# Kernel tuning notes

Measured on AMD Instinct MI355X. Metric: run time of the kernel, lower is better.

The kernel has to match this reference:

```python
import jax, jax.numpy as jnp
import numpy as np

N_NODES = 50000
N_EDGES = 500000
NEG_SLOPE = 0.2


def gat_conv(h, src, dst, W, attn_l, attn_r, bias, activation):
    """DGL-style GATConv (feat_drop=attn_drop=0, no residual).
    h: [N, F_in]; W: [F_in, H*D]; attn_l/attn_r: [H, D]; bias: [H*D].
    Returns [N, H, D]."""
    H, D = attn_l.shape
    feat = (h @ W).reshape(-1, H, D)                      # [N, H, D]
    el = (feat * attn_l).sum(-1)                          # [N, H]
    er = (feat * attn_r).sum(-1)                          # [N, H]
    e = jax.nn.leaky_relu(el[src] + er[dst], NEG_SLOPE)   # [E, H] edge logits
    # edge softmax over incoming edges of each dst node
    emax = jax.ops.segment_max(e, dst, num_segments=N_NODES)
    emax = jnp.where(jnp.isfinite(emax), emax, 0.0)       # guard zero in-degree
    ee = jnp.exp(e - emax[dst])                           # [E, H]
    denom = jax.ops.segment_sum(ee, dst, num_segments=N_NODES)
    alpha = ee / jnp.maximum(denom[dst], 1e-9)            # [E, H]
    # weighted scatter-aggregate of source features
    out = jax.ops.segment_sum(feat[src] * alpha[..., None], dst,
                              num_segments=N_NODES)       # [N, H, D]
    out = out + bias.reshape(1, H, D)
    return activation(out) if activation is not None else out


def setup_inputs() -> dict:
    key = jax.random.key(0)
    ks = jax.random.split(key, 20)
    in0, in1, hid, heads, ncls = 256, 128, 64, 8, 10

    def xn(k, shape):
        fan = shape[0] + (shape[1] if len(shape) > 1 else shape[0])
        return jax.random.normal(k, shape, jnp.float32) * np.float32(np.sqrt(2.0 / fan)) * 1.414

    inp = {
        "feat0": jax.random.normal(ks[0], (30000, in0), jnp.float32),
        "feat1": jax.random.normal(ks[1], (20000, in1), jnp.float32),
        "fc0_w": xn(ks[2], (in0, hid)), "fc0_b": jnp.zeros((hid,), jnp.float32),
        "fc1_w": xn(ks[3], (in1, hid)), "fc1_b": jnp.zeros((hid,), jnp.float32),
        "W0": xn(ks[4], (hid, heads * hid)),
        "al0": xn(ks[5], (heads, hid)), "ar0": xn(ks[6], (heads, hid)),
        "b0": jnp.zeros((heads * hid,), jnp.float32),
        "W1": xn(ks[7], (heads * hid, heads * hid)),
        "al1": xn(ks[8], (heads, hid)), "ar1": xn(ks[9], (heads, hid)),
        "b1": jnp.zeros((heads * hid,), jnp.float32),
        "W2": xn(ks[10], (heads * hid, 1 * ncls)),
        "al2": xn(ks[11], (1, ncls)), "ar2": xn(ks[12], (1, ncls)),
        "b2": jnp.zeros((ncls,), jnp.float32),
        "edge_index": jax.random.randint(ks[13], (2, N_EDGES), 0, N_NODES, jnp.int64
                                         if jax.config.jax_enable_x64 else jnp.int32),
    }
    return inp


def reference(feat0, feat1, fc0_w, fc0_b, fc1_w, fc1_b,
              W0, al0, ar0, b0, W1, al1, ar1, b1, W2, al2, ar2, b2,
              edge_index):
    src, dst = edge_index[0], edge_index[1]
    # per-type linear projection then concat along node axis
    h = jnp.concatenate([feat0 @ fc0_w + fc0_b, feat1 @ fc1_w + fc1_b], axis=0)
    h = gat_conv(h, src, dst, W0, al0, ar0, b0, jax.nn.elu).reshape(N_NODES, -1)
    h = gat_conv(h, src, dst, W1, al1, ar1, b1, jax.nn.elu).reshape(N_NODES, -1)
    logits = gat_conv(h, src, dst, W2, al2, ar2, b2, None).mean(axis=1)  # [N, ncls]
    return logits
```

## Files before the change

### kernel.cpp

```cpp
#include <hip/hip_runtime.h>
#include <hip/hip_bf16.h>

#define N_NODES 50000
#define N_EDGES 500000
#define HEADS 8
#define HID 64
#define HD 512
#define NCLS 10
#define M_PAD 50048

typedef __bf16 bf16x8 __attribute__((ext_vector_type(8)));
typedef float  f32x4  __attribute__((ext_vector_type(4)));
typedef unsigned short us8v __attribute__((ext_vector_type(8)));

__device__ __forceinline__ float bf2f(unsigned short u) {
    union { unsigned int i; float f; } v; v.i = ((unsigned int)u) << 16; return v.f;
}
__device__ __forceinline__ unsigned short f2bf(float x) {
    __hip_bfloat16 b = __float2bfloat16(x);
    return *reinterpret_cast<unsigned short*>(&b);
}

#define GLD_LDS16(g, l) __builtin_amdgcn_global_load_lds( \
    (__attribute__((address_space(1))) void*)(g),         \
    (__attribute__((address_space(3))) void*)(l), 16, 0, 0)

#define T0_TILES 469
#define T1_TILES 313
__global__ __launch_bounds__(256) void fc_gemm(const float* __restrict__ A0,
                                               const float* __restrict__ B0,
                                               const float* __restrict__ bias0,
                                               const float* __restrict__ A1,
                                               const float* __restrict__ B1,
                                               const float* __restrict__ bias1,
                                               __hip_bfloat16* __restrict__ Cb) {
    __shared__ float As[16][68];
    __shared__ float Bs[16][68];
    int bid = blockIdx.x;
    const float* A; const float* B; const float* bias;
    int M, K, row_off, m0;
    if (bid < T0_TILES) { A = A0; B = B0; bias = bias0; M = 30000; K = 256; row_off = 0;     m0 = bid * 64; }
    else                { A = A1; B = B1; bias = bias1; M = 20000; K = 128; row_off = 30000; m0 = (bid - T0_TILES) * 64; }
    int tid = threadIdx.x;
    int tx = tid & 15, ty = tid >> 4;
    float acc[4][4] = {};
    int arow = tid >> 2;
    int akq  = (tid & 3) * 4;
    int brow = tid >> 4;
    int bcol = (tid & 15) * 4;
    for (int k0 = 0; k0 < K; k0 += 16) {
        int m = m0 + arow;
        float4 av = make_float4(0.f, 0.f, 0.f, 0.f);
        if (m < M) av = *(const float4*)(A + (size_t)m * K + k0 + akq);
        As[akq + 0][arow] = av.x; As[akq + 1][arow] = av.y;
        As[akq + 2][arow] = av.z; As[akq + 3][arow] = av.w;
        float4 bv = *(const float4*)(B + (size_t)(k0 + brow) * 64 + bcol);
        *(float4*)(&Bs[brow][bcol]) = bv;
        __syncthreads();
#pragma unroll
        for (int k = 0; k < 16; k++) {
            float4 a = *(const float4*)(&As[k][ty * 4]);
            float4 b = *(const float4*)(&Bs[k][tx * 4]);
            float av4[4] = {a.x, a.y, a.z, a.w};
            float bv4[4] = {b.x, b.y, b.z, b.w};
#pragma unroll
            for (int i = 0; i < 4; i++)
#pragma unroll
                for (int j = 0; j < 4; j++) acc[i][j] += av4[i] * bv4[j];
        }
        __syncthreads();
    }
#pragma unroll
    for (int i = 0; i < 4; i++) {
        int m = m0 + ty * 4 + i;
        if (m < M) {
#pragma unroll
            for (int j = 0; j < 4; j++) {
                int col = tx * 4 + j;
                Cb[(size_t)(row_off + m) * 64 + col] = __float2bfloat16(acc[i][j] + bias[col]);
            }
        }
    }
}

#define NBLK_SCAN 196

__global__ void count_kernel(const int* __restrict__ dst, int* __restrict__ cnt) {
    int t = blockIdx.x * blockDim.x + threadIdx.x;
    if (t < N_EDGES) atomicAdd(&cnt[dst[t]], 1);
}

__global__ void scan_part(const int* __restrict__ cnt, int* __restrict__ part) {
    __shared__ int s[256];
    int i = blockIdx.x * 256 + threadIdx.x;
    s[threadIdx.x] = (i < N_NODES) ? cnt[i] : 0;
    __syncthreads();
    for (int off = 128; off; off >>= 1) {
        if (threadIdx.x < off) s[threadIdx.x] += s[threadIdx.x + off];
        __syncthreads();
    }
    if (threadIdx.x == 0) part[blockIdx.x] = s[0];
}

__global__ void scan_offs(int* __restrict__ part) {
    __shared__ int s[256];
    int tid = threadIdx.x;
    int v = (tid < NBLK_SCAN) ? part[tid] : 0;
    s[tid] = v;
    __syncthreads();
    for (int off = 1; off < 256; off <<= 1) {
        int x = (tid >= off) ? s[tid - off] : 0;
        __syncthreads();
        s[tid] += x;
        __syncthreads();
    }
    if (tid < NBLK_SCAN) part[tid] = s[tid] - v;
}

__global__ void scan_apply(const int* __restrict__ cnt, const int* __restrict__ part,
                           int* __restrict__ rp, int* __restrict__ cur) {
    __shared__ int s[256];
    int tid = threadIdx.x;
    int i = blockIdx.x * 256 + tid;
    int v = (i < N_NODES) ? cnt[i] : 0;
    s[tid] = v;
    __syncthreads();
    for (int off = 1; off < 256; off <<= 1) {
        int x = (tid >= off) ? s[tid - off] : 0;
        __syncthreads();
        s[tid] += x;
        __syncthreads();
    }
    if (i < N_NODES) {
        int excl = s[tid] - v + part[blockIdx.x];
        rp[i] = excl; cur[i] = excl;
    }
    if (i == 0) rp[N_NODES] = N_EDGES;
}

__global__ void scatter_kernel(const int* __restrict__ src, const int* __restrict__ dst,
                               int* __restrict__ cursor, int* __restrict__ src_sorted) {
    int t = blockIdx.x * blockDim.x + threadIdx.x;
    if (t >= N_EDGES) return;
    int pos = atomicAdd(&cursor[dst[t]], 1);
    src_sorted[pos] = src[t];
}

__global__ void wtrans(const float* __restrict__ W, __hip_bfloat16* __restrict__ Wt,
                       int Kdim, int Ndim) {
    int t = blockIdx.x * blockDim.x + threadIdx.x;
    if (t >= Kdim * Ndim) return;
    int n = t / Kdim, k = t - n * Kdim;
    Wt[t] = __float2bfloat16(W[k * Ndim + n]);
}

__global__ __launch_bounds__(256) void gemm_mfma(const ushort* __restrict__ A,
                                                 const ushort* __restrict__ Bt,
                                                 __hip_bfloat16* __restrict__ Cb,
                                                 const float* __restrict__ al,
                                                 const float* __restrict__ ar,
                                                 float* __restrict__ el,
                                                 float* __restrict__ er,
                                                 int M, int N, int K) {
    __shared__ ushort Asl[128 * 32];
    __shared__ ushort Bsl[128 * 32];
    int t = threadIdx.x;
    int m0 = blockIdx.y * 128, n0 = blockIdx.x * 128;
    int lane = t & 63;
    int w = t >> 6;
    int wm = (w & 1) * 64, wn = (w >> 1) * 64;
    int l15 = lane & 15, quad = lane >> 4;
    f32x4 acc[4][4];
#pragma unroll
    for (int i = 0; i < 4; i++)
#pragma unroll
        for (int j = 0; j < 4; j++) acc[i][j] = (f32x4){0.f, 0.f, 0.f, 0.f};

    int fb0 = t * 16;
    int fb1 = fb0 + 4096;
    int row0 = fb0 >> 6, kg0 = ((fb0 >> 4) & 3) ^ (row0 & 3);
    int row1 = fb1 >> 6, kg1 = ((fb1 >> 4) & 3) ^ (row1 & 3);

    for (int k0 = 0; k0 < K; k0 += 32) {
        GLD_LDS16(A + (size_t)(m0 + row0) * K + k0 + kg0 * 8, (char*)Asl + fb0);
        GLD_LDS16(A + (size_t)(m0 + row1) * K + k0 + kg1 * 8, (char*)Asl + fb1);
        GLD_LDS16(Bt + (size_t)(n0 + row0) * K + k0 + kg0 * 8, (char*)Bsl + fb0);
        GLD_LDS16(Bt + (size_t)(n0 + row1) * K + k0 + kg1 * 8, (char*)Bsl + fb1);
        __syncthreads();
        bf16x8 af[4], bfr[4];
#pragma unroll
        for (int i = 0; i < 4; i++) {
            int r = wm + i * 16 + l15;
            int kg = quad ^ (r & 3);
            af[i] = *(const bf16x8*)(Asl + r * 32 + kg * 8);
        }
#pragma unroll
        for (int j = 0; j < 4; j++) {
            int r = wn + j * 16 + l15;
            int kg = quad ^ (r & 3);
            bfr[j] = *(const bf16x8*)(Bsl + r * 32 + kg * 8);
        }
#pragma unroll
        for (int i = 0; i < 4; i++)
#pragma unroll
            for (int j = 0; j < 4; j++)
                acc[i][j] = __builtin_amdgcn_mfma_f32_16x16x32_bf16(af[i], bfr[j], acc[i][j], 0, 0, 0);
        __syncthreads();
    }
#pragma unroll
    for (int i = 0; i < 4; i++) {
        int rbase = m0 + wm + i * 16 + quad * 4;
#pragma unroll
        for (int j = 0; j < 4; j++) {
            int col = n0 + wn + j * 16 + l15;
#pragma unroll
            for (int r = 0; r < 4; r++) {
                int row = rbase + r;
                if (row < M) Cb[(size_t)row * N + col] = __float2bfloat16(acc[i][j][r]);
            }
        }
    }
    int h = (n0 + wn) >> 6;
    float alv[4], arv[4];
#pragma unroll
    for (int j = 0; j < 4; j++) {
        alv[j] = al[h * 64 + j * 16 + l15];
        arv[j] = ar[h * 64 + j * 16 + l15];
    }
#pragma unroll
    for (int i = 0; i < 4; i++) {
#pragma unroll
        for (int r = 0; r < 4; r++) {
            float sl = 0.f, sr = 0.f;
#pragma unroll
            for (int j = 0; j < 4; j++) {
                float v = acc[i][j][r];
                sl += v * alv[j]; sr += v * arv[j];
            }
#pragma unroll
            for (int mk = 1; mk < 16; mk <<= 1) {
                sl += __shfl_xor(sl, mk);
                sr += __shfl_xor(sr, mk);
            }
            int row = m0 + wm + i * 16 + quad * 4 + r;
            if (l15 == 0 && row < M) {
                el[row * HEADS + h] = sl;
                er[row * HEADS + h] = sr;
            }
        }
    }
}

__global__ __launch_bounds__(256) void attn_agg(
        const int* __restrict__ rp, const int* __restrict__ srcs,
        const float* __restrict__ el, const float* __restrict__ er,
        const ushort* __restrict__ feat, const float* __restrict__ bias,
        ushort* __restrict__ out) {
    __shared__ float aS[4][592];
    __shared__ int   sS[4][64];
    int lane = threadIdx.x & 63;
    int w    = threadIdx.x >> 6;
    int n    = blockIdx.x * 4 + w;
    int s0 = rp[n], s1 = rp[n + 1];
    int deg = s1 - s0;
    float er8[8];
    {
        f32x4 a = *(const f32x4*)(er + (size_t)n * 8);
        f32x4 b = *(const f32x4*)(er + (size_t)n * 8 + 4);
        er8[0]=a[0]; er8[1]=a[1]; er8[2]=a[2]; er8[3]=a[3];
        er8[4]=b[0]; er8[5]=b[1]; er8[6]=b[2]; er8[7]=b[3];
    }
    bool fast = (deg <= 64);
    if (fast) {
        bool act = lane < deg;
        int sp = act ? srcs[s0 + lane] : 0;
        sS[w][lane] = sp;
        f32x4 ea = {0.f,0.f,0.f,0.f}, eb = {0.f,0.f,0.f,0.f};
        if (act) {
            ea = *(const f32x4*)(el + (size_t)sp * 8);
            eb = *(const f32x4*)(el + (size_t)sp * 8 + 4);
        }
        float e8[8] = {ea[0],ea[1],ea[2],ea[3],eb[0],eb[1],eb[2],eb[3]};
        float m8[8], s8[8];
#pragma unroll
        for (int h = 0; h < 8; h++) {
            float e = e8[h] + er8[h];
            e = e > 0.f ? e : 0.2f * e;
            e8[h] = act ? e : -1e30f;
        }
#pragma unroll
        for (int h = 0; h < 8; h++) {
            float mm = e8[h];
#pragma unroll
            for (int mk = 1; mk < 64; mk <<= 1) mm = fmaxf(mm, __shfl_xor(mm, mk));
            m8[h] = mm;
        }
#pragma unroll
        for (int h = 0; h < 8; h++) {
            float pv = act ? __expf(e8[h] - m8[h]) : 0.f;
            aS[w][lane * 9 + h] = pv;
            float ss = pv;
#pragma unroll
            for (int mk = 1; mk < 64; mk <<= 1) ss += __shfl_xor(ss, mk);
            s8[h] = ss;
        }
        if (lane == 0) {
#pragma unroll
            for (int h = 0; h < 8; h++) aS[w][576 + h] = 1.f / fmaxf(s8[h], 1e-9f);
        }
    } else {
        float m8[8], s8[8];
#pragma unroll
        for (int h = 0; h < 8; h++) { m8[h] = -1e30f; s8[h] = 0.f; }
        for (int base = s0; base < s1; base += 64) {
            bool act = base + lane < s1;
            int sp = act ? srcs[base + lane] : 0;
            f32x4 ea = {0.f,0.f,0.f,0.f}, eb = {0.f,0.f,0.f,0.f};
            if (act) {
                ea = *(const f32x4*)(el + (size_t)sp * 8);
                eb = *(const f32x4*)(el + (size_t)sp * 8 + 4);
            }
            float ev[8] = {ea[0],ea[1],ea[2],ea[3],eb[0],eb[1],eb[2],eb[3]};
#pragma unroll
            for (int h = 0; h < 8; h++) {
                float e = ev[h] + er8[h];
                e = e > 0.f ? e : 0.2f * e;
                e = act ? e : -1e30f;
                float cm = e;
#pragma unroll
                for (int mk = 1; mk < 64; mk <<= 1) cm = fmaxf(cm, __shfl_xor(cm, mk));
                float nm = fmaxf(m8[h], cm);
                float pv = act ? __expf(e - nm) : 0.f;
#pragma unroll
                for (int mk = 1; mk < 64; mk <<= 1) pv += __shfl_xor(pv, mk);
                s8[h] = s8[h] * __expf(m8[h] - nm) + pv;
                m8[h] = nm;
            }
        }
        if (lane == 0) {
#pragma unroll
            for (int h = 0; h < 8; h++) {
                aS[w][576 + h] = 1.f / fmaxf(s8[h], 1e-9f);
                aS[w][584 + h] = m8[h];
            }
        }
    }
    __syncthreads();
    int hh = lane >> 3, d0 = (lane & 7) * 8;
    float inv_l = aS[w][576 + hh];
    float acc[8] = {0.f,0.f,0.f,0.f,0.f,0.f,0.f,0.f};
    const ushort* colbase = feat + hh * 64 + d0;
    if (fast) {
        for (int p = 0; p < deg; p++) {
            int sp = sS[w][p];
            float a = aS[w][p * 9 + hh] * inv_l;
            us8v f = *(const us8v*)(colbase + (size_t)sp * HD);
#pragma unroll
            for (int j = 0; j < 8; j++) acc[j] += a * bf2f(f[j]);
        }
    } else {
        float m_l   = aS[w][584 + hh];
        float ern_l = er[(size_t)n * 8 + hh];
        for (int p = s0; p < s1; p++) {
            int sp = srcs[p];
            float e = el[(size_t)sp * 8 + hh] + ern_l;
            e = e > 0.f ? e : 0.2f * e;
            float a = __expf(e - m_l) * inv_l;
            us8v f = *(const us8v*)(colbase + (size_t)sp * HD);
#pragma unroll
            for (int j = 0; j < 8; j++) acc[j] += a * bf2f(f[j]);
        }
    }
    float4 b0v = *(const float4*)(bias + lane * 8);
    float4 b1v = *(const float4*)(bias + lane * 8 + 4);
    float bb[8] = {b0v.x,b0v.y,b0v.z,b0v.w,b1v.x,b1v.y,b1v.z,b1v.w};
    us8v o;
#pragma unroll
    for (int j = 0; j < 8; j++) {
        float x = acc[j] + bb[j];
        x = x > 0.f ? x : __expf(x) - 1.f;
        o[j] = f2bf(x);
    }
    *(us8v*)(out + (size_t)n * HD + lane * 8) = o;
}

__global__ __launch_bounds__(256) void gemm_n10v2(
        const ushort* __restrict__ A, const float* __restrict__ B,
        const float* __restrict__ al2, const float* __restrict__ ar2,
        float* __restrict__ C, float* __restrict__ el, float* __restrict__ er) {
    __shared__ float Bs[512 * 11];
    int t = threadIdx.x;
    for (int i = t; i < 512 * NCLS; i += 256) {
        int k = i / NCLS, c = i - k * NCLS;
        Bs[k * 11 + c] = B[i];
    }
    __syncthreads();
    int lane = t & 63;
    int m = blockIdx.x * 4 + (t >> 6);
    float acc[NCLS];
#pragma unroll
    for (int c = 0; c < NCLS; c++) acc[c] = 0.f;
    const ushort* a = A + (size_t)m * HD;
#pragma unroll
    for (int j = 0; j < 8; j++) {
        float av = bf2f(a[j * 64 + lane]);
        const float* br = Bs + (j * 64 + lane) * 11;
#pragma unroll
        for (int c = 0; c < NCLS; c++) acc[c] += av * br[c];
    }
#pragma unroll
    for (int c = 0; c < NCLS; c++)
#pragma unroll
        for (int mk = 1; mk < 64; mk <<= 1) acc[c] += __shfl_xor(acc[c], mk);
    if (lane == 0) {
        float e1 = 0.f, e2 = 0.f;
#pragma unroll
        for (int c = 0; c < NCLS; c++) { e1 += acc[c] * al2[c]; e2 += acc[c] * ar2[c]; }
        el[m] = e1; er[m] = e2;
#pragma unroll
        for (int c = 0; c < NCLS; c++) C[(size_t)m * NCLS + c] = acc[c];
    }
}

__global__ __launch_bounds__(256) void attn2_agg2(
        const int* __restrict__ rp, const int* __restrict__ srcs,
        const float* __restrict__ el, const float* __restrict__ er,
        const float* __restrict__ feat2, const float* __restrict__ b2,
        float* __restrict__ out) {
    int lane = threadIdx.x & 63;
    int n = blockIdx.x * 4 + (threadIdx.x >> 6);
    int s0 = rp[n], s1 = rp[n + 1], deg = s1 - s0;
    float ern = er[n];
    float facc[NCLS];
#pragma unroll
    for (int c = 0; c < NCLS; c++) facc[c] = 0.f;
    if (deg <= 64) {
        bool act = lane < deg;
        int sp = act ? srcs[s0 + lane] : 0;
        float e = act ? el[sp] + ern : 0.f;
        e = e > 0.f ? e : 0.2f * e;
        if (!act) e = -1e30f;
        float mm = e;
#pragma unroll
        for (int mk = 1; mk < 64; mk <<= 1) mm = fmaxf(mm, __shfl_xor(mm, mk));
        float pv = act ? __expf(e - mm) : 0.f;
        float ss = pv;
#pragma unroll
        for (int mk = 1; mk < 64; mk <<= 1) ss += __shfl_xor(ss, mk);
        float a = pv / fmaxf(ss, 1e-9f);
        if (act) {
#pragma unroll
            for (int c = 0; c < NCLS; c++) facc[c] = a * feat2[(size_t)sp * NCLS + c];
        }
    } else {
        float mm = -1e30f, ssum = 0.f;
        for (int base = s0; base < s1; base += 64) {
            bool act = base + lane < s1;
            int sp = act ? srcs[base + lane] : 0;
            float e = act ? el[sp] + ern : 0.f;
            e = e > 0.f ? e : 0.2f * e;
            if (!act) e = -1e30f;
            float cm = e;
#pragma unroll
            for (int mk = 1; mk < 64; mk <<= 1) cm = fmaxf(cm, __shfl_xor(cm, mk));
            float nm = fmaxf(mm, cm);
            float pv = act ? __expf(e - nm) : 0.f;
#pragma unroll
            for (int mk = 1; mk < 64; mk <<= 1) pv += __shfl_xor(pv, mk);
            ssum = ssum * __expf(mm - nm) + pv;
            mm = nm;
        }
        float inv = 1.f / fmaxf(ssum, 1e-9f);
        for (int base = s0; base < s1; base += 64) {
            bool act = base + lane < s1;
            int sp = act ? srcs[base + lane] : 0;
            float e = act ? el[sp] + ern : 0.f;
            e = e > 0.f ? e : 0.2f * e;
            float a = act ? __expf(e - mm) * inv : 0.f;
            if (act) {
#pragma unroll
                for (int c = 0; c < NCLS; c++) facc[c] += a * feat2[(size_t)sp * NCLS + c];
            }
        }
    }
#pragma unroll
    for (int c = 0; c < NCLS; c++)
#pragma unroll
        for (int mk = 1; mk < 64; mk <<= 1) facc[c] += __shfl_xor(facc[c], mk);
    if (lane == 0) {
#pragma unroll
        for (int c = 0; c < NCLS; c++) out[(size_t)n * NCLS + c] = facc[c] + b2[c];
    }
}

extern "C" void kernel_launch(void* const* d_in, const int* in_sizes, int n_in,
                              void* d_out, int out_size, void* d_ws, size_t ws_size,
                              hipStream_t stream) {
    const float* feat0 = (const float*)d_in[0];
    const float* feat1 = (const float*)d_in[1];
    const float* fc0_w = (const float*)d_in[2];
    const float* fc0_b = (const float*)d_in[3];
    const float* fc1_w = (const float*)d_in[4];
    const float* fc1_b = (const float*)d_in[5];
    const float* W0    = (const float*)d_in[6];
    const float* al0   = (const float*)d_in[7];
    const float* ar0   = (const float*)d_in[8];
    const float* b0    = (const float*)d_in[9];
    const float* W1    = (const float*)d_in[10];
    const float* al1   = (const float*)d_in[11];
    const float* ar1   = (const float*)d_in[12];
    const float* b1    = (const float*)d_in[13];
    const float* W2    = (const float*)d_in[14];
    const float* al2   = (const float*)d_in[15];
    const float* ar2   = (const float*)d_in[16];
    const float* b2    = (const float*)d_in[17];
    const int* eidx    = (const int*)d_in[18];
    const int* src = eidx;
    const int* dst = eidx + N_EDGES;
    float* out = (float*)d_out;

    char* ws = (char*)d_ws;
    size_t off = 0;
    auto alloc = [&](size_t bytes) { size_t o = off; off = (off + bytes + 255) & ~(size_t)255; return o; };

    __hip_bfloat16* featAbf = (__hip_bfloat16*)(ws + alloc((size_t)M_PAD * HD * 2));
    __hip_bfloat16* aggbf   = (__hip_bfloat16*)(ws + alloc((size_t)M_PAD * HD * 2));
    __hip_bfloat16* h0bf    = (__hip_bfloat16*)(ws + alloc((size_t)M_PAD * 64 * 2));
    float*          feat2   = (float*)(ws + alloc((size_t)N_NODES * NCLS * 4));
    float*          el      = (float*)(ws + alloc((size_t)N_NODES * HEADS * 4));
    float*          er      = (float*)(ws + alloc((size_t)N_NODES * HEADS * 4));
    int*            cnt     = (int*)  (ws + alloc((size_t)N_NODES * 4));
    int*            rp      = (int*)  (ws + alloc((size_t)(N_NODES + 1) * 4));
    int*            cur     = (int*)  (ws + alloc((size_t)N_NODES * 4));
    int*            srcs    = (int*)  (ws + alloc((size_t)N_EDGES * 4));
    int*            part    = (int*)  (ws + alloc(1024));
    __hip_bfloat16* W0t     = (__hip_bfloat16*)(ws + alloc(512 * 64 * 2));
    __hip_bfloat16* W1t     = (__hip_bfloat16*)(ws + alloc(512 * 512 * 2));

    fc_gemm<<<T0_TILES + T1_TILES, 256, 0, stream>>>(feat0, fc0_w, fc0_b,
                                                     feat1, fc1_w, fc1_b, h0bf);
    wtrans<<<(512 * 64 + 255) / 256, 256, 0, stream>>>(W0, W0t, 64, 512);
    wtrans<<<(512 * 512 + 255) / 256, 256, 0, stream>>>(W1, W1t, 512, 512);

    hipMemsetAsync(cnt, 0, N_NODES * sizeof(int), stream);
    count_kernel<<<(N_EDGES + 255) / 256, 256, 0, stream>>>(dst, cnt);
    scan_part<<<NBLK_SCAN, 256, 0, stream>>>(cnt, part);
    scan_offs<<<1, 256, 0, stream>>>(part);
    scan_apply<<<NBLK_SCAN, 256, 0, stream>>>(cnt, part, rp, cur);
    scatter_kernel<<<(N_EDGES + 255) / 256, 256, 0, stream>>>(src, dst, cur, srcs);

    dim3 ggrid(HD / 128, M_PAD / 128);

    gemm_mfma<<<ggrid, 256, 0, stream>>>((const ushort*)h0bf, (const ushort*)W0t, featAbf,
                                         al0, ar0, el, er, N_NODES, HD, 64);
    attn_agg<<<N_NODES / 4, 256, 0, stream>>>(rp, srcs, el, er, (const ushort*)featAbf,
                                              b0, (ushort*)aggbf);

    gemm_mfma<<<ggrid, 256, 0, stream>>>((const ushort*)aggbf, (const ushort*)W1t, featAbf,
                                         al1, ar1, el, er, N_NODES, HD, HD);
    attn_agg<<<N_NODES / 4, 256, 0, stream>>>(rp, srcs, el, er, (const ushort*)featAbf,
                                              b1, (ushort*)aggbf);

    gemm_n10v2<<<N_NODES / 4, 256, 0, stream>>>((const ushort*)aggbf, W2, al2, ar2,
                                                feat2, el, er);
    attn2_agg2<<<N_NODES / 4, 256, 0, stream>>>(rp, srcs, el, er, feat2, b2, out);
}
```

Before: 544.6 us.

## Switch intermediates to fp16, packed fp16 aggregation, K=64 GEMM tiles, fused wtrans

Replaces the bf16 intermediate storage with fp16 and moves the MFMA GEMM to the f16 instruction. The GEMM now loads 64-wide K tiles with an 8-way XOR swizzle, halving the number of loop iterations and barriers. The attention aggregation accumulates in packed fp16 vectors and folds the softmax normalisation into the stored weights, which cuts per-edge conversion and FMA work. The two weight-transpose launches are merged into one. Accumulating in fp16 risks precision loss and overflow over high-degree nodes.

```diff
diff --git a/kernel.cpp b/kernel.cpp
--- a/kernel.cpp
+++ b/kernel.cpp
@@ -1,5 +1,6 @@
 #include <hip/hip_runtime.h>
 #include <hip/hip_bf16.h>
+#include <hip/hip_fp16.h>
 
 #define N_NODES 50000
 #define N_EDGES 500000
@@ -9,17 +10,9 @@
 #define NCLS 10
 #define M_PAD 50048
 
-typedef __bf16 bf16x8 __attribute__((ext_vector_type(8)));
-typedef float  f32x4  __attribute__((ext_vector_type(4)));
-typedef unsigned short us8v __attribute__((ext_vector_type(8)));
-
-__device__ __forceinline__ float bf2f(unsigned short u) {
-    union { unsigned int i; float f; } v; v.i = ((unsigned int)u) << 16; return v.f;
-}
-__device__ __forceinline__ unsigned short f2bf(float x) {
-    __hip_bfloat16 b = __float2bfloat16(x);
-    return *reinterpret_cast<unsigned short*>(&b);
-}
+typedef _Float16 f16x8 __attribute__((ext_vector_type(8)));
+typedef _Float16 h8v   __attribute__((ext_vector_type(8)));
+typedef float    f32x4 __attribute__((ext_vector_type(4)));
 
 #define GLD_LDS16(g, l) __builtin_amdgcn_global_load_lds( \
     (__attribute__((address_space(1))) void*)(g),         \
@@ -33,7 +26,7 @@
                                                const float* __restrict__ A1,
                                                const float* __restrict__ B1,
                                                const float* __restrict__ bias1,
-                                               __hip_bfloat16* __restrict__ Cb) {
+                                               _Float16* __restrict__ Cb) {
     __shared__ float As[16][68];
     __shared__ float Bs[16][68];
     int bid = blockIdx.x;
@@ -77,7 +70,7 @@
 #pragma unroll
             for (int j = 0; j < 4; j++) {
                 int col = tx * 4 + j;
-                Cb[(size_t)(row_off + m) * 64 + col] = __float2bfloat16(acc[i][j] + bias[col]);
+                Cb[(size_t)(row_off + m) * 64 + col] = (_Float16)(acc[i][j] + bias[col]);
             }
         }
     }
@@ -146,24 +139,30 @@
     src_sorted[pos] = src[t];
 }
 
-__global__ void wtrans(const float* __restrict__ W, __hip_bfloat16* __restrict__ Wt,
-                       int Kdim, int Ndim) {
+__global__ void wtrans(const float* __restrict__ W0, const float* __restrict__ W1,
+                       _Float16* __restrict__ W0t, _Float16* __restrict__ W1t) {
     int t = blockIdx.x * blockDim.x + threadIdx.x;
-    if (t >= Kdim * Ndim) return;
-    int n = t / Kdim, k = t - n * Kdim;
-    Wt[t] = __float2bfloat16(W[k * Ndim + n]);
-}
-
-__global__ __launch_bounds__(256) void gemm_mfma(const ushort* __restrict__ A,
-                                                 const ushort* __restrict__ Bt,
-                                                 __hip_bfloat16* __restrict__ Cb,
+    if (t < 64 * 512) {
+        int n = t >> 6, k = t & 63;
+        W0t[t] = (_Float16)W0[k * 512 + n];
+    } else {
+        int u = t - 64 * 512;
+        if (u >= 512 * 512) return;
+        int n = u >> 9, k = u & 511;
+        W1t[u] = (_Float16)W1[k * 512 + n];
+    }
+}
+
+__global__ __launch_bounds__(256) void gemm_mfma(const _Float16* __restrict__ A,
+                                                 const _Float16* __restrict__ Bt,
+                                                 _Float16* __restrict__ Cb,
                                                  const float* __restrict__ al,
                                                  const float* __restrict__ ar,
                                                  float* __restrict__ el,
                                                  float* __restrict__ er,
                                                  int M, int N, int K) {
-    __shared__ ushort Asl[128 * 32];
-    __shared__ ushort Bsl[128 * 32];
+    __shared__ _Float16 Asl[128 * 64];
+    __shared__ _Float16 Bsl[128 * 64];
     int t = threadIdx.x;
     int m0 = blockIdx.y * 128, n0 = blockIdx.x * 128;
     int lane = t & 63;
@@ -176,35 +175,44 @@
 #pragma unroll
         for (int j = 0; j < 4; j++) acc[i][j] = (f32x4){0.f, 0.f, 0.f, 0.f};
 
-    int fb0 = t * 16;
-    int fb1 = fb0 + 4096;
-    int row0 = fb0 >> 6, kg0 = ((fb0 >> 4) & 3) ^ (row0 & 3);
-    int row1 = fb1 >> 6, kg1 = ((fb1 >> 4) & 3) ^ (row1 & 3);
-
-    for (int k0 = 0; k0 < K; k0 += 32) {
-        GLD_LDS16(A + (size_t)(m0 + row0) * K + k0 + kg0 * 8, (char*)Asl + fb0);
-        GLD_LDS16(A + (size_t)(m0 + row1) * K + k0 + kg1 * 8, (char*)Asl + fb1);
-        GLD_LDS16(Bt + (size_t)(n0 + row0) * K + k0 + kg0 * 8, (char*)Bsl + fb0);
-        GLD_LDS16(Bt + (size_t)(n0 + row1) * K + k0 + kg1 * 8, (char*)Bsl + fb1);
-        __syncthreads();
-        bf16x8 af[4], bfr[4];
-#pragma unroll
-        for (int i = 0; i < 4; i++) {
-            int r = wm + i * 16 + l15;
-            int kg = quad ^ (r & 3);
-            af[i] = *(const bf16x8*)(Asl + r * 32 + kg * 8);
-        }
-#pragma unroll
-        for (int j = 0; j < 4; j++) {
-            int r = wn + j * 16 + l15;
-            int kg = quad ^ (r & 3);
-            bfr[j] = *(const bf16x8*)(Bsl + r * 32 + kg * 8);
-        }
-#pragma unroll
-        for (int i = 0; i < 4; i++)
-#pragma unroll
-            for (int j = 0; j < 4; j++)
-                acc[i][j] = __builtin_amdgcn_mfma_f32_16x16x32_bf16(af[i], bfr[j], acc[i][j], 0, 0, 0);
+    int rowS[4], kgS[4], fbS[4];
+#pragma unroll
+    for (int ps = 0; ps < 4; ps++) {
+        int fb = t * 16 + ps * 4096;
+        int row = fb >> 7;
+        int kg = ((fb >> 4) & 7) ^ (row & 7);
+        rowS[ps] = row; kgS[ps] = kg; fbS[ps] = fb;
+    }
+
+    for (int k0 = 0; k0 < K; k0 += 64) {
+#pragma unroll
+        for (int ps = 0; ps < 4; ps++)
+            GLD_LDS16(A + (size_t)(m0 + rowS[ps]) * K + k0 + kgS[ps] * 8, (char*)Asl + fbS[ps]);
+#pragma unroll
+        for (int ps = 0; ps < 4; ps++)
+            GLD_LDS16(Bt + (size_t)(n0 + rowS[ps]) * K + k0 + kgS[ps] * 8, (char*)Bsl + fbS[ps]);
+        __syncthreads();
+#pragma unroll
+        for (int s = 0; s < 2; s++) {
+            f16x8 af[4], bfr[4];
+#pragma unroll
+            for (int i = 0; i < 4; i++) {
+                int r = wm + i * 16 + l15;
+                int g = ((s << 2) | quad) ^ (r & 7);
+                af[i] = *(const f16x8*)(Asl + r * 64 + g * 8);
+            }
+#pragma unroll
+            for (int j = 0; j < 4; j++) {
+                int r = wn + j * 16 + l15;
+                int g = ((s << 2) | quad) ^ (r & 7);
+                bfr[j] = *(const f16x8*)(Bsl + r * 64 + g * 8);
+            }
+#pragma unroll
+            for (int i = 0; i < 4; i++)
+#pragma unroll
+                for (int j = 0; j < 4; j++)
+                    acc[i][j] = __builtin_amdgcn_mfma_f32_16x16x32_f16(af[i], bfr[j], acc[i][j], 0, 0, 0);
+        }
         __syncthreads();
     }
 #pragma unroll
@@ -216,7 +224,7 @@
 #pragma unroll
             for (int r = 0; r < 4; r++) {
                 int row = rbase + r;
-                if (row < M) Cb[(size_t)row * N + col] = __float2bfloat16(acc[i][j][r]);
+                if (row < M) Cb[(size_t)row * N + col] = (_Float16)acc[i][j][r];
             }
         }
     }
@@ -254,8 +262,8 @@
 __global__ __launch_bounds__(256) void attn_agg(
         const int* __restrict__ rp, const int* __restrict__ srcs,
         const float* __restrict__ el, const float* __restrict__ er,
-        const ushort* __restrict__ feat, const float* __restrict__ bias,
-        ushort* __restrict__ out) {
+        const _Float16* __restrict__ feat, const float* __restrict__ bias,
+        _Float16* __restrict__ out) {
     __shared__ float aS[4][592];
     __shared__ int   sS[4][64];
     int lane = threadIdx.x & 63;
@@ -281,7 +289,6 @@
             eb = *(const f32x4*)(el + (size_t)sp * 8 + 4);
         }
         float e8[8] = {ea[0],ea[1],ea[2],ea[3],eb[0],eb[1],eb[2],eb[3]};
-        float m8[8], s8[8];
 #pragma unroll
         for (int h = 0; h < 8; h++) {
             float e = e8[h] + er8[h];
@@ -293,20 +300,11 @@
             float mm = e8[h];
 #pragma unroll
             for (int mk = 1; mk < 64; mk <<= 1) mm = fmaxf(mm, __shfl_xor(mm, mk));
-            m8[h] = mm;
-        }
-#pragma unroll
-        for (int h = 0; h < 8; h++) {
-            float pv = act ? __expf(e8[h] - m8[h]) : 0.f;
-            aS[w][lane * 9 + h] = pv;
+            float pv = act ? __expf(e8[h] - mm) : 0.f;
             float ss = pv;
 #pragma unroll
             for (int mk = 1; mk < 64; mk <<= 1) ss += __shfl_xor(ss, mk);
-            s8[h] = ss;
-        }
-        if (lane == 0) {
-#pragma unroll
-            for (int h = 0; h < 8; h++) aS[w][576 + h] = 1.f / fmaxf(s8[h], 1e-9f);
+            aS[w][lane * 9 + h] = pv * (1.f / fmaxf(ss, 1e-9f));
         }
     } else {
         float m8[8], s8[8];
@@ -347,45 +345,46 @@
     }
     __syncthreads();
     int hh = lane >> 3, d0 = (lane & 7) * 8;
-    float inv_l = aS[w][576 + hh];
-    float acc[8] = {0.f,0.f,0.f,0.f,0.f,0.f,0.f,0.f};
-    const ushort* colbase = feat + hh * 64 + d0;
+    h8v acc8 = {(_Float16)0, (_Float16)0, (_Float16)0, (_Float16)0,
+                (_Float16)0, (_Float16)0, (_Float16)0, (_Float16)0};
+    const _Float16* colbase = feat + hh * 64 + d0;
     if (fast) {
         for (int p = 0; p < deg; p++) {
             int sp = sS[w][p];
-            float a = aS[w][p * 9 + hh] * inv_l;
-            us8v f = *(const us8v*)(colbase + (size_t)sp * HD);
-#pragma unroll
-            for (int j = 0; j < 8; j++) acc[j] += a * bf2f(f[j]);
+            _Float16 ah = (_Float16)aS[w][p * 9 + hh];
+            h8v a8 = {ah, ah, ah, ah, ah, ah, ah, ah};
+            h8v f = *(const h8v*)(colbase + (size_t)sp * HD);
+            acc8 += a8 * f;
         }
     } else {
+        float inv_l = aS[w][576 + hh];
         float m_l   = aS[w][584 + hh];
         float ern_l = er[(size_t)n * 8 + hh];
         for (int p = s0; p < s1; p++) {
             int sp = srcs[p];
             float e = el[(size_t)sp * 8 + hh] + ern_l;
             e = e > 0.f ? e : 0.2f * e;
-            float a = __expf(e - m_l) * inv_l;
-            us8v f = *(const us8v*)(colbase + (size_t)sp * HD);
-#pragma unroll
-            for (int j = 0; j < 8; j++) acc[j] += a * bf2f(f[j]);
+            _Float16 ah = (_Float16)(__expf(e - m_l) * inv_l);
+            h8v a8 = {ah, ah, ah, ah, ah, ah, ah, ah};
+            h8v f = *(const h8v*)(colbase + (size_t)sp * HD);
+            acc8 += a8 * f;
         }
     }
     float4 b0v = *(const float4*)(bias + lane * 8);
     float4 b1v = *(const float4*)(bias + lane * 8 + 4);
     float bb[8] = {b0v.x,b0v.y,b0v.z,b0v.w,b1v.x,b1v.y,b1v.z,b1v.w};
-    us8v o;
+    h8v o;
 #pragma unroll
     for (int j = 0; j < 8; j++) {
-        float x = acc[j] + bb[j];
+        float x = (float)acc8[j] + bb[j];
         x = x > 0.f ? x : __expf(x) - 1.f;
-        o[j] = f2bf(x);
-    }
-    *(us8v*)(out + (size_t)n * HD + lane * 8) = o;
+        o[j] = (_Float16)x;
+    }
+    *(h8v*)(out + (size_t)n * HD + lane * 8) = o;
 }
 
 __global__ __launch_bounds__(256) void gemm_n10v2(
-        const ushort* __restrict__ A, const float* __restrict__ B,
+        const _Float16* __restrict__ A, const float* __restrict__ B,
         const float* __restrict__ al2, const float* __restrict__ ar2,
         float* __restrict__ C, float* __restrict__ el, float* __restrict__ er) {
     __shared__ float Bs[512 * 11];
@@ -400,10 +399,10 @@
     float acc[NCLS];
 #pragma unroll
     for (int c = 0; c < NCLS; c++) acc[c] = 0.f;
-    const ushort* a = A + (size_t)m * HD;
+    const _Float16* a = A + (size_t)m * HD;
 #pragma unroll
     for (int j = 0; j < 8; j++) {
-        float av = bf2f(a[j * 64 + lane]);
+        float av = (float)a[j * 64 + lane];
         const float* br = Bs + (j * 64 + lane) * 11;
 #pragma unroll
         for (int c = 0; c < NCLS; c++) acc[c] += av * br[c];
@@ -523,24 +522,23 @@
     size_t off = 0;
     auto alloc = [&](size_t bytes) { size_t o = off; off = (off + bytes + 255) & ~(size_t)255; return o; };
 
-    __hip_bfloat16* featAbf = (__hip_bfloat16*)(ws + alloc((size_t)M_PAD * HD * 2));
-    __hip_bfloat16* aggbf   = (__hip_bfloat16*)(ws + alloc((size_t)M_PAD * HD * 2));
-    __hip_bfloat16* h0bf    = (__hip_bfloat16*)(ws + alloc((size_t)M_PAD * 64 * 2));
-    float*          feat2   = (float*)(ws + alloc((size_t)N_NODES * NCLS * 4));
-    float*          el      = (float*)(ws + alloc((size_t)N_NODES * HEADS * 4));
-    float*          er      = (float*)(ws + alloc((size_t)N_NODES * HEADS * 4));
-    int*            cnt     = (int*)  (ws + alloc((size_t)N_NODES * 4));
-    int*            rp      = (int*)  (ws + alloc((size_t)(N_NODES + 1) * 4));
-    int*            cur     = (int*)  (ws + alloc((size_t)N_NODES * 4));
-    int*            srcs    = (int*)  (ws + alloc((size_t)N_EDGES * 4));
-    int*            part    = (int*)  (ws + alloc(1024));
-    __hip_bfloat16* W0t     = (__hip_bfloat16*)(ws + alloc(512 * 64 * 2));
-    __hip_bfloat16* W1t     = (__hip_bfloat16*)(ws + alloc(512 * 512 * 2));
+    _Float16* featA = (_Float16*)(ws + alloc((size_t)M_PAD * HD * 2));
+    _Float16* aggh  = (_Float16*)(ws + alloc((size_t)M_PAD * HD * 2));
+    _Float16* h0h   = (_Float16*)(ws + alloc((size_t)M_PAD * 64 * 2));
+    float*    feat2 = (float*)(ws + alloc((size_t)N_NODES * NCLS * 4));
+    float*    el    = (float*)(ws + alloc((size_t)N_NODES * HEADS * 4));
+    float*    er    = (float*)(ws + alloc((size_t)N_NODES * HEADS * 4));
+    int*      cnt   = (int*)  (ws + alloc((size_t)N_NODES * 4));
+    int*      rp    = (int*)  (ws + alloc((size_t)(N_NODES + 1) * 4));
+    int*      cur   = (int*)  (ws + alloc((size_t)N_NODES * 4));
+    int*      srcs  = (int*)  (ws + alloc((size_t)N_EDGES * 4));
+    int*      part  = (int*)  (ws + alloc(1024));
+    _Float16* W0t   = (_Float16*)(ws + alloc(512 * 64 * 2));
+    _Float16* W1t   = (_Float16*)(ws + alloc(512 * 512 * 2));
 
     fc_gemm<<<T0_TILES + T1_TILES, 256, 0, stream>>>(feat0, fc0_w, fc0_b,
-                                                     feat1, fc1_w, fc1_b, h0bf);
-    wtrans<<<(512 * 64 + 255) / 256, 256, 0, stream>>>(W0, W0t, 64, 512);
-    wtrans<<<(512 * 512 + 255) / 256, 256, 0, stream>>>(W1, W1t, 512, 512);
+                                                     feat1, fc1_w, fc1_b, h0h);
+    wtrans<<<(64 * 512 + 512 * 512 + 255) / 256, 256, 0, stream>>>(W0, W1, W0t, W1t);
 
     hipMemsetAsync(cnt, 0, N_NODES * sizeof(int), stream);
     count_kernel<<<(N_EDGES + 255) / 256, 256, 0, stream>>>(dst, cnt);
@@ -551,17 +549,14 @@
 
     dim3 ggrid(HD / 128, M_PAD / 128);
 
-    gemm_mfma<<<ggrid, 256, 0, stream>>>((const ushort*)h0bf, (const ushort*)W0t, featAbf,
-                                         al0, ar0, el, er, N_NODES, HD, 64);
-    attn_agg<<<N_NODES / 4, 256, 0, stream>>>(rp, srcs, el, er, (const ushort*)featAbf,
-                                              b0, (ushort*)aggbf);
-
-    gemm_mfma<<<ggrid, 256, 0, stream>>>((const ushort*)aggbf, (const ushort*)W1t, featAbf,
-                                         al1, ar1, el, er, N_NODES, HD, HD);
-    attn_agg<<<N_NODES / 4, 256, 0, stream>>>(rp, srcs, el, er, (const ushort*)featAbf,
-                                              b1, (ushort*)aggbf);
-
-    gemm_n10v2<<<N_NODES / 4, 256, 0, stream>>>((const ushort*)aggbf, W2, al2, ar2,
-                                                feat2, el, er);
+    gemm_mfma<<<ggrid, 256, 0, stream>>>(h0h, W0t, featA, al0, ar0, el, er,
+                                         N_NODES, HD, 64);
+    attn_agg<<<N_NODES / 4, 256, 0, stream>>>(rp, srcs, el, er, featA, b0, aggh);
+
+    gemm_mfma<<<ggrid, 256, 0, stream>>>(aggh, W1t, featA, al1, ar1, el, er,
+                                         N_NODES, HD, HD);
+    attn_agg<<<N_NODES / 4, 256, 0, stream>>>(rp, srcs, el, er, featA, b1, aggh);
+
+    gemm_n10v2<<<N_NODES / 4, 256, 0, stream>>>(aggh, W2, al2, ar2, feat2, el, er);
     attn2_agg2<<<N_NODES / 4, 256, 0, stream>>>(rp, srcs, el, er, feat2, b2, out);
 }
```

Result: slower. 561.2 us (+3.0%).
